# Kernel optimization log

Hardware: AMD Instinct MI355X
Metric: run time of the kernel (lower is better)

## Reference

```python
import jax, jax.numpy as jnp
import numpy as np

# dims: n_embd == dim_att == C, head_size N, heads H = C//N
B, T, C = 4, 2048, 2048
HS = 64
H = C // HS
D_MIX = 32
D_DECAY = 128
LAYER_ID, N_LAYER = 12, 24
LN_EPS = 1e-5


def setup_inputs() -> dict:
    key = jax.random.key(0)
    ks = jax.random.split(key, 12)
    r01 = LAYER_ID / (N_LAYER - 1)
    r1a0 = 1.0 - LAYER_ID / N_LAYER
    ddd = np.arange(C, dtype=np.float64) / C
    decay_speed = -6.0 + 5.0 * (np.arange(C, dtype=np.float64) / (C - 1)) ** (0.7 + 1.3 * r01)
    zig = ((np.arange(C) + 1) % 3 - 1) * 0.1
    faaaa = r01 * (1.0 - np.arange(C, dtype=np.float64) / (C - 1)) + zig
    uni = lambda k, sh, s: jax.random.uniform(k, sh, jnp.float32, -s, s)
    return dict(
        x_in=jax.random.normal(ks[0], (B, T, C), jnp.float32),
        shift_state=jax.random.normal(ks[1], (B, C), jnp.float32),
        wkv_state=jnp.zeros((B, H, HS, HS), jnp.float32),
        time_maa_r=jnp.asarray(1.0 - ddd ** (0.5 * r1a0), jnp.float32).reshape(1, 1, C),
        time_maa_k=jnp.asarray(1.0 - ddd ** r1a0, jnp.float32).reshape(1, 1, C),
        time_maa_v=jnp.asarray(1.0 - (ddd ** r1a0 + 0.3 * r01), jnp.float32).reshape(1, 1, C),
        time_maa_v2=jnp.asarray(1.0 - (ddd ** r1a0 + 0.3 * r01), jnp.float32).reshape(1, 1, C),
        time_maa_w1=uni(ks[2], (C, 4 * D_MIX), 0.01),  # zeros in true init; small values for nontrivial test
        time_maa_w2=uni(ks[3], (4, D_MIX, C), 0.01),
        time_maa_w=jnp.asarray(1.0 - ddd ** r1a0, jnp.float32).reshape(1, 1, C),
        time_maa_w_w1=uni(ks[4], (C, D_MIX), 0.01),
        time_maa_w_w2=uni(ks[5], (D_MIX, C), 0.01),
        time_decay=jnp.asarray(decay_speed, jnp.float32).reshape(1, 1, C),
        time_decay_w1=uni(ks[6], (C, D_DECAY), 0.01),
        time_decay_w2=uni(ks[7], (D_DECAY, C), 0.01),
        time_faaaa=jnp.asarray(faaaa, jnp.float32).reshape(H, HS),
        time_receptance=uni(ks[8], (C,), 1.0),
        time_key=uni(ks[9], (C,), 1.0),
        value_w=jax.random.normal(ks[10], (C, C), jnp.float32) / np.sqrt(C),
        output_w=jax.random.normal(ks[11], (C, C), jnp.float32) / np.sqrt(C),
        ln_gamma=jnp.ones((C,), jnp.float32),
        ln_beta=jnp.zeros((C,), jnp.float32),
    )


def _wkv6(r, k, v, decay, u, state):
    # r,k,v,decay: (B,T,H,N); u: (H,N); state: (B,H,N,N) [key i, value j]
    def step(S, inp):
        rt, kt, vt, dt = inp  # each (B,H,N)
        kv = kt[..., :, None] * vt[..., None, :]  # (B,H,N,N)
        y = jnp.einsum('bhi,bhij->bhj', rt, S + u[None, :, :, None] * kv)
        S = dt[..., None] * S + kv
        return S, y
    tb = lambda a: jnp.swapaxes(a, 0, 1)  # (B,T,...) -> (T,B,...)
    S_fin, ys = jax.lax.scan(step, state, (tb(r), tb(k), tb(v), tb(decay)))
    return tb(ys), S_fin  # (B,T,H,N), (B,H,N,N)


def reference(x_in, shift_state, wkv_state, time_maa_r, time_maa_k, time_maa_v,
              time_maa_v2, time_maa_w1, time_maa_w2, time_maa_w, time_maa_w_w1,
              time_maa_w_w2, time_decay, time_decay_w1, time_decay_w2, time_faaaa,
              time_receptance, time_key, value_w, output_w, ln_gamma, ln_beta):
    Bs, Ts, Cs = x_in.shape
    Hn, Nn = time_faaaa.shape
    # token-shift LoRA mixing coefficients (4, B, T, C)
    xxx = jnp.tanh(x_in @ time_maa_w1).reshape(Bs, Ts, 4, -1)
    mix = jnp.einsum('btfd,fdc->fbtc', xxx, time_maa_w2)
    x = x_in @ value_w.T  # value projection (B,T,C)
    shift_out = x[:, -1]
    dxprev = jnp.concatenate([shift_state[:, None, :], x[:, :-1]], axis=1) - x
    # data-dependent decay
    mw = jnp.tanh(x @ time_maa_w_w1) @ time_maa_w_w2
    xw = x + dxprev * (time_maa_w + mw)
    w = time_decay + jnp.tanh(xw @ time_decay_w1) @ time_decay_w2  # (B,T,C)
    mr, mk, mv, mv2 = mix[0], mix[1], mix[2], mix[3]
    xv = x + dxprev * (time_maa_v + mv)
    xr = x + dxprev * (time_maa_r + mr)
    xk = x + dxprev * (time_maa_k + mk)
    xv2 = x + dxprev * (time_maa_v2 + mv2)
    v = xv
    r = xr * time_receptance
    k = xk * time_key
    v2 = xv2
    decay = jnp.exp(-jnp.exp(w))  # per-channel decay in (0,1)
    k = k * (1.0 - decay)
    u = jnp.zeros_like(time_faaaa)
    hv = lambda a: a.reshape(Bs, Ts, Hn, Nn)
    y, S_fin = _wkv6(hv(r), hv(k), hv(v), hv(decay), u, wkv_state)
    y = y.reshape(Bs, Ts, Cs) + v2
    # LayerNorm over last dim
    mu = y.mean(-1, keepdims=True)
    var = ((y - mu) ** 2).mean(-1, keepdims=True)
    y = (y - mu) * jax.lax.rsqrt(var + LN_EPS) * ln_gamma + ln_beta
    out = y @ output_w.T
    return out
```

## Files before the change

kernel.cpp:

```cpp
#include <hip/hip_runtime.h>


#define Cdim 2048
#define Tdim 2048

using short8 = __attribute__((ext_vector_type(8))) short;
using f32x4  = __attribute__((ext_vector_type(4))) float;
using us4    = __attribute__((ext_vector_type(4))) unsigned short;
typedef unsigned short ushort_t;

__device__ __forceinline__ float b2f(unsigned short h) {
    union { unsigned int u; float f; } x; x.u = ((unsigned int)h) << 16; return x.f;
}
__device__ __forceinline__ unsigned short f2b(float f) {
    union { float f; unsigned int u; } x; x.f = f;
    unsigned int r = x.u + 0x7fffu + ((x.u >> 16) & 1u);
    return (unsigned short)(r >> 16);
}

__device__ __forceinline__ void gload16(const void* g, void* l) {
    __builtin_amdgcn_global_load_lds(
        (__attribute__((address_space(1))) void*)g,
        (__attribute__((address_space(3))) void*)l, 16, 0, 0);
}

__global__ __launch_bounds__(256) void prep_k(
    const float* __restrict__ x_in, const float* __restrict__ valw,
    const float* __restrict__ outw,
    ushort_t* __restrict__ xinB, ushort_t* __restrict__ valwB,
    ushort_t* __restrict__ outwB,
    const float* __restrict__ w1,  const float* __restrict__ ww1,
    const float* __restrict__ dw1, const float* __restrict__ dw2,
    const float* __restrict__ ww2, const float* __restrict__ w2,
    ushort_t* __restrict__ w1T,  ushort_t* __restrict__ ww1T,
    ushort_t* __restrict__ dw1T, ushort_t* __restrict__ dw2T,
    ushort_t* __restrict__ ww2T, ushort_t* __restrict__ w2T)
{
    size_t g = (size_t)blockIdx.x * 256 + threadIdx.x;
    if (g < 6291456) {
        const float* src; ushort_t* dst; size_t e;
        if (g < 4194304)      { src = x_in; dst = xinB;  e = g; }
        else if (g < 5242880) { src = valw; dst = valwB; e = g - 4194304; }
        else                  { src = outw; dst = outwB; e = g - 5242880; }
        const float4 v = ((const float4*)src)[e];
        us4 o; o.x = f2b(v.x); o.y = f2b(v.y); o.z = f2b(v.z); o.w = f2b(v.w);
        ((us4*)dst)[e] = o;
        return;
    }
    int idx = (int)(g - 6291456);
    if (idx < 262144) { int r = idx >> 7, c = idx & 127; w1T[c * 2048 + r] = f2b(w1[idx]); return; }
    idx -= 262144;
    if (idx < 65536)  { int r = idx >> 5, c = idx & 31;  ww1T[c * 2048 + r] = f2b(ww1[idx]); return; }
    idx -= 65536;
    if (idx < 262144) { int r = idx >> 7, c = idx & 127; dw1T[c * 2048 + r] = f2b(dw1[idx]); return; }
    idx -= 262144;
    if (idx < 262144) { int r = idx >> 11, c = idx & 2047; dw2T[c * 128 + r] = f2b(dw2[idx]); return; }
    idx -= 262144;
    if (idx < 65536)  { int r = idx >> 11, c = idx & 2047; ww2T[c * 32 + r] = f2b(ww2[idx]); return; }
    idx -= 65536;
    { int f = idx >> 16, rem = idx & 65535; int r = rem >> 11, c = rem & 2047;
      w2T[f * 65536 + c * 32 + r] = f2b(w2[idx]); }
}

template <int MODE>
__global__ __launch_bounds__(512, 2) void gemm256_k(
    const ushort_t* __restrict__ A,
    const ushort_t* __restrict__ Bw,
    ushort_t* __restrict__ outB,
    float* __restrict__ outF)
{
    __shared__ __align__(16) ushort_t lds[65536];

    const int tid  = threadIdx.x;
    const int wave = tid >> 6, lane = tid & 63;
    const int wm = wave >> 2, wn = wave & 3;
    const int fr = lane & 15, quad = lane >> 4;
    const int og8 = (((lane & 7) ^ ((lane >> 3) & 7)) * 8);

    const int id  = blockIdx.x;
    const int swz = (id & 7) * 32 + (id >> 3);
    const int mbase = (swz >> 3) * 256;
    const int nbase = (swz & 7) * 256;

    f32x4 acc[8][4];
#pragma unroll
    for (int i = 0; i < 8; ++i)
#pragma unroll
        for (int j = 0; j < 4; ++j)
#pragma unroll
            for (int r = 0; r < 4; ++r) acc[i][j][r] = 0.f;

    auto stage_half = [&](const ushort_t* __restrict__ G, int growb,
                          int dstb, int kt) {
#pragma unroll
        for (int i = 0; i < 2; ++i) {
            const int rh = i * 64 + wave * 8 + (lane >> 3);
            gload16(G + (size_t)(growb + rh) * Cdim + kt * 64 + og8,
                    &lds[dstb + (i * 512 + wave * 64) * 8]);
        }
    };

    short8 afr[4][2], bfr[2][2];

    auto LOADA = [&](int p, int mo) {
#pragma unroll
        for (int mi = 0; mi < 4; ++mi)
#pragma unroll
            for (int k = 0; k < 2; ++k) {
                const int row = wm * 128 + (mo + mi) * 16 + fr;
                afr[mi][k] = *(const short8*)
                    &lds[p + row * 64 + (((k * 4 + quad) ^ (fr & 7)) * 8)];
            }
    };
    auto LOADB = [&](int p, int no) {
#pragma unroll
        for (int ni = 0; ni < 2; ++ni)
#pragma unroll
            for (int k = 0; k < 2; ++k) {
                const int row = wn * 64 + (no + ni) * 16 + fr;
                bfr[ni][k] = *(const short8*)
                    &lds[32768 + p + row * 64 + (((k * 4 + quad) ^ (fr & 7)) * 8)];
            }
    };
    auto MFMA16 = [&](int mo, int no) {
        __builtin_amdgcn_s_setprio(1);
#pragma unroll
        for (int mi = 0; mi < 4; ++mi)
#pragma unroll
            for (int ni = 0; ni < 2; ++ni)
#pragma unroll
                for (int k = 0; k < 2; ++k)
                    acc[mo + mi][no + ni] = __builtin_amdgcn_mfma_f32_16x16x32_bf16(
                        afr[mi][k], bfr[ni][k], acc[mo + mi][no + ni], 0, 0, 0);
        __builtin_amdgcn_s_setprio(0);
    };

    stage_half(A,  mbase,       0,            0);
    stage_half(A,  mbase + 128, 8192,         0);
    stage_half(Bw, nbase,       32768,        0);
    stage_half(Bw, nbase + 128, 32768 + 8192, 0);

#pragma unroll 2
    for (int t = 0; t < 32; ++t) {
        const int p  = (t & 1) * 16384;
        const int q  = 16384 - p;
        const int kn = (t < 31) ? t + 1 : t;

        asm volatile("s_waitcnt vmcnt(0)\n\ts_barrier" ::: "memory");
        LOADA(p, 0); LOADB(p, 0);
        stage_half(A, mbase,       q,        kn);
        stage_half(A, mbase + 128, q + 8192, kn);
        asm volatile("s_barrier" ::: "memory");
        asm volatile("s_waitcnt lgkmcnt(0)" ::: "memory");
        MFMA16(0, 0);

        asm volatile("s_barrier" ::: "memory");
        LOADB(p, 2);
        stage_half(Bw, nbase,       32768 + q,        kn);
        stage_half(Bw, nbase + 128, 32768 + q + 8192, kn);
        asm volatile("s_barrier" ::: "memory");
        asm volatile("s_waitcnt lgkmcnt(0)" ::: "memory");
        MFMA16(0, 2);

        asm volatile("s_barrier" ::: "memory");
        LOADA(p, 4);
        asm volatile("s_barrier" ::: "memory");
        asm volatile("s_waitcnt lgkmcnt(0)" ::: "memory");
        MFMA16(4, 2);

        asm volatile("s_barrier" ::: "memory");
        LOADB(p, 0);
        asm volatile("s_barrier" ::: "memory");
        asm volatile("s_waitcnt lgkmcnt(0)" ::: "memory");
        MFMA16(4, 0);
    }

    const int row0 = mbase + wm * 128 + quad * 4;
    const int col0 = nbase + wn * 64 + fr;
#pragma unroll
    for (int mi = 0; mi < 8; ++mi)
#pragma unroll
        for (int ni = 0; ni < 4; ++ni)
#pragma unroll
            for (int r = 0; r < 4; ++r) {
                const int row = row0 + mi * 16 + r;
                const int col = col0 + ni * 16;
                const size_t idx = (size_t)row * Cdim + col;
                if constexpr (MODE == 2) outB[idx] = f2b(acc[mi][ni][r]);
                else                     outF[idx] = acc[mi][ni][r];
            }
}

__global__ __launch_bounds__(256) void mix5_k(
    const ushort_t* __restrict__ xxx,
    const ushort_t* __restrict__ mwpre,
    const ushort_t* __restrict__ w2T,
    const ushort_t* __restrict__ ww2T,
    const ushort_t* __restrict__ xB,
    const float*    __restrict__ shiftS,
    const float* __restrict__ maa_r, const float* __restrict__ maa_k,
    const float* __restrict__ maa_v, const float* __restrict__ maa_v2,
    const float* __restrict__ maa_w,
    const float* __restrict__ recep, const float* __restrict__ tkey,
    ushort_t* __restrict__ mR,  ushort_t* __restrict__ mK,
    ushort_t* __restrict__ mV,  ushort_t* __restrict__ mV2,
    ushort_t* __restrict__ xwB)
{
    __shared__ __align__(16) ushort_t xs[129 * 136];
    __shared__ __align__(16) ushort_t abuf[128 * 32];
    __shared__ __align__(16) ushort_t bbuf[128 * 32];

    const int tid  = threadIdx.x;
    const int wave = tid >> 6, lane = tid & 63;
    const int wm = wave >> 1, wn = wave & 1;
    const int fr = lane & 15, quad = lane >> 4;

    const int mbase = blockIdx.x * 128;
    const int nbase = blockIdx.y * 128;
    const int b  = mbase >> 11;
    const int t0 = mbase & 2047;

#pragma unroll
    for (int it = 0; it < 8; ++it) {
        const int idx = it * 256 + tid;
        const int r = idx >> 4, c8 = (idx & 15) * 8;
        *(short8*)&xs[(r + 1) * 136 + c8] =
            *(const short8*)&xB[(size_t)(mbase + r) * Cdim + nbase + c8];
    }
    if (tid < 128)
        xs[tid] = (t0 > 0) ? xB[(size_t)(mbase - 1) * Cdim + nbase + tid]
                           : f2b(shiftS[(size_t)b * Cdim + nbase + tid]);

    const ushort_t* asrc[5] = {xxx, xxx + 32, xxx + 64, xxx + 96, mwpre};
    const int       alda[5] = {128, 128, 128, 128, 32};
    const ushort_t* bsrc[5] = {w2T, w2T + 65536, w2T + 131072, w2T + 196608, ww2T};
    const float*    cvec[5] = {maa_r, maa_k, maa_v, maa_v2, maa_w};
    const float*    cmul[5] = {recep, tkey, nullptr, nullptr, nullptr};
    ushort_t*       outs[5] = {mR, mK, mV, mV2, xwB};

    auto stageAB = [&](int o) {
#pragma unroll
        for (int i = 0; i < 2; ++i) {
            const int slot = i * 256 + tid;
            const int r = slot >> 2, oct = slot & 3;
            const int sw = ((oct ^ (r & 3)) * 8);
            gload16(asrc[o] + (size_t)(mbase + r) * alda[o] + sw, &abuf[slot * 8]);
            gload16(bsrc[o] + (size_t)(nbase + r) * 32 + sw,      &bbuf[slot * 8]);
        }
    };

    stageAB(0);
    __syncthreads();

    const int row0l = wm * 64 + quad * 4;
    const int col0l = wn * 64 + fr;

#pragma unroll
    for (int o = 0; o < 5; ++o) {
        short8 af[4], bf[4];
#pragma unroll
        for (int mi = 0; mi < 4; ++mi) {
            const int r = wm * 64 + mi * 16 + fr;
            af[mi] = *(const short8*)&abuf[r * 32 + ((quad ^ (r & 3)) * 8)];
        }
#pragma unroll
        for (int ni = 0; ni < 4; ++ni) {
            const int r = wn * 64 + ni * 16 + fr;
            bf[ni] = *(const short8*)&bbuf[r * 32 + ((quad ^ (r & 3)) * 8)];
        }
        asm volatile("s_waitcnt lgkmcnt(0)" ::: "memory");
        __builtin_amdgcn_sched_barrier(0);
        asm volatile("s_barrier" ::: "memory");
        if (o < 4) stageAB(o + 1);

        f32x4 acc[4][4];
#pragma unroll
        for (int mi = 0; mi < 4; ++mi)
#pragma unroll
            for (int ni = 0; ni < 4; ++ni) {
#pragma unroll
                for (int r = 0; r < 4; ++r) acc[mi][ni][r] = 0.f;
                acc[mi][ni] = __builtin_amdgcn_mfma_f32_16x16x32_bf16(
                    af[mi], bf[ni], acc[mi][ni], 0, 0, 0);
            }

        const float* cv = cvec[o];
        const float* cm = cmul[o];
        ushort_t* op = outs[o];
#pragma unroll
        for (int mi = 0; mi < 4; ++mi)
#pragma unroll
            for (int ni = 0; ni < 4; ++ni)
#pragma unroll
                for (int r = 0; r < 4; ++r) {
                    const int lr = row0l + mi * 16 + r;
                    const int lc = col0l + ni * 16;
                    const int col = nbase + lc;
                    const float x  = b2f(xs[(lr + 1) * 136 + lc]);
                    const float xp = (lr == 0 && t0 == 0)
                                         ? shiftS[(size_t)b * Cdim + col]
                                         : b2f(xs[lr * 136 + lc]);
                    float val = x + (xp - x) * (cv[col] + acc[mi][ni][r]);
                    if (cm) val *= cm[col];
                    op[(size_t)(mbase + lr) * Cdim + col] = f2b(val);
                }
        if (o < 4)
            asm volatile("s_waitcnt vmcnt(0)\n\ts_barrier" ::: "memory");
    }
}

template <int MODE>
__global__ __launch_bounds__(256) void gemm_bt_k(
    const ushort_t* __restrict__ A, int lda,
    const ushort_t* __restrict__ Bw, int ldb,
    int N, int K,
    ushort_t* __restrict__ outB, int ldc,
    const float* __restrict__ cvec,
    ushort_t* __restrict__ inplace)
{
    __shared__ __align__(16) ushort_t At[128 * 32];
    __shared__ __align__(16) ushort_t Bt[128 * 32];

    const int tid  = threadIdx.x;
    const int wave = tid >> 6, lane = tid & 63;
    const int wm = wave >> 1, wn = wave & 1;
    const int fr = lane & 15, quad = lane >> 4;
    const int cr = lane >> 2;
    const int cc = (lane & 3) * 8;

    f32x4 acc[4][4];
#pragma unroll
    for (int i = 0; i < 4; ++i)
#pragma unroll
        for (int j = 0; j < 4; ++j)
#pragma unroll
            for (int r = 0; r < 4; ++r) acc[i][j][r] = 0.f;

    const int mbase = blockIdx.x * 128;
    const int nbase = blockIdx.y * 128;

    for (int k0 = 0; k0 < K; k0 += 32) {
        __syncthreads();
#pragma unroll
        for (int c2 = 0; c2 < 2; ++c2) {
            const int q  = wave * 2 + c2;
            const int ar = mbase + q * 16 + cr;
            gload16(A + (size_t)ar * lda + k0 + cc, &At[q * 512]);
            int br = nbase + q * 16 + cr;
            br = br < N ? br : N - 1;
            gload16(Bw + (size_t)br * ldb + k0 + cc, &Bt[q * 512]);
        }
        __syncthreads();

        short8 af[4], bfr[4];
#pragma unroll
        for (int mi = 0; mi < 4; ++mi)
            af[mi] = *(const short8*)&At[(wm * 64 + mi * 16 + fr) * 32 + quad * 8];
#pragma unroll
        for (int ni = 0; ni < 4; ++ni)
            bfr[ni] = *(const short8*)&Bt[(wn * 64 + ni * 16 + fr) * 32 + quad * 8];
#pragma unroll
        for (int mi = 0; mi < 4; ++mi)
#pragma unroll
            for (int ni = 0; ni < 4; ++ni)
                acc[mi][ni] = __builtin_amdgcn_mfma_f32_16x16x32_bf16(
                    af[mi], bfr[ni], acc[mi][ni], 0, 0, 0);
    }

    const int row0 = mbase + wm * 64 + quad * 4;
    const int col0 = nbase + wn * 64 + fr;
#pragma unroll
    for (int mi = 0; mi < 4; ++mi) {
#pragma unroll
        for (int ni = 0; ni < 4; ++ni) {
            const int col = col0 + ni * 16;
#pragma unroll
            for (int r = 0; r < 4; ++r) {
                const int row = row0 + mi * 16 + r;
                const float v = acc[mi][ni][r];
                const size_t idx = (size_t)row * ldc + col;
                if constexpr (MODE == 1) {
                    if (col < N) outB[idx] = f2b(tanhf(v));
                } else {
                    const float w  = cvec[col] + v;
                    const float ew = __expf(w);
                    outB[idx] = f2b(ew);
                    inplace[idx] = f2b(b2f(inplace[idx]) * (1.f - __expf(-ew)));
                }
            }
        }
    }
}

__global__ __launch_bounds__(64) void wkv_chunk_a(
    const ushort_t* __restrict__ ewB,
    ushort_t* rB, ushort_t* kB,
    const ushort_t* __restrict__ vB,
    ushort_t* __restrict__ uOut, float* __restrict__ dtot)
{
    const int c = blockIdx.x, h = blockIdx.y, b = blockIdx.z;
    const int lane = threadIdx.x;
    const int fr = lane & 15, quad = lane >> 4;
    __shared__ __align__(16) ushort_t kTT[64 * 40];
    __shared__ __align__(16) ushort_t vT [64 * 40];

    const size_t rowbase = ((size_t)b * Tdim + c * 32) * Cdim + h * 64;

    float Lrun = 0.f;
    for (int t = 0; t < 32; ++t) {
        const size_t off = rowbase + (size_t)t * Cdim + lane;
        const float e  = b2f(ewB[off]);
        const float rv = b2f(rB[off]);
        const float kv = b2f(kB[off]);
        const ushort_t rT = f2b(rv * __expf(Lrun));
        const ushort_t kT = f2b(kv * __expf(e - Lrun));
        rB[off] = rT;
        kB[off] = kT;
        kTT[lane * 40 + t] = kT;
        vT [lane * 40 + t] = vB[off];
        Lrun -= e;
    }
    const int slab = (b * 32 + h) * 64 + c;
    dtot[(size_t)slab * 64 + lane] = __expf(Lrun);
    __syncthreads();

    short8 af[4], bf[4];
#pragma unroll
    for (int mj = 0; mj < 4; ++mj)
        af[mj] = *(const short8*)&vT[(mj * 16 + fr) * 40 + quad * 8];
#pragma unroll
    for (int ni = 0; ni < 4; ++ni)
        bf[ni] = *(const short8*)&kTT[(ni * 16 + fr) * 40 + quad * 8];

    ushort_t* uo = uOut + (size_t)slab * 4096;
#pragma unroll
    for (int mj = 0; mj < 4; ++mj) {
#pragma unroll
        for (int ni = 0; ni < 4; ++ni) {
            f32x4 acc = {0.f, 0.f, 0.f, 0.f};
            acc = __builtin_amdgcn_mfma_f32_16x16x32_bf16(af[mj], bf[ni], acc, 0, 0, 0);
#pragma unroll
            for (int r = 0; r < 4; ++r) {
                const int j = mj * 16 + quad * 4 + r;
                const int i = ni * 16 + fr;
                uo[j * 64 + i] = f2b(acc[r]);
            }
        }
    }
}

__global__ __launch_bounds__(256) void wkv_scan_b(
    ushort_t* __restrict__ slabs, const float* __restrict__ dtot,
    const float* __restrict__ s0)
{
    const int jhi = blockIdx.x, h = blockIdx.y, b = blockIdx.z;
    const int tid = threadIdx.x;
    const int ip = tid & 31, jl = tid >> 5;
    const int i0 = ip * 2;
    const int j  = jhi * 8 + jl;
    const size_t bh = (size_t)(b * 32 + h);
    const size_t base = bh * 64;

    __shared__ float dsh[64 * 64];
    for (int e = tid; e < 4096; e += 256) dsh[e] = dtot[base * 64 + e];

    const float* sp = s0 + bh * 4096;
    float sa = sp[i0 * 64 + j];
    float sb = sp[(i0 + 1) * 64 + j];
    __syncthreads();

    unsigned int* up =
        (unsigned int*)(slabs + base * 4096 + (size_t)j * 64 + i0);
#pragma unroll 8
    for (int c = 0; c < 64; ++c) {
        const unsigned int u = up[(size_t)c * 2048];
        const float2 dt = *(const float2*)&dsh[c * 64 + i0];
        const unsigned int pre =
            (unsigned int)f2b(sa) | ((unsigned int)f2b(sb) << 16);
        sa = dt.x * (sa + b2f((ushort_t)(u & 0xffffu)));
        sb = dt.y * (sb + b2f((ushort_t)(u >> 16)));
        up[(size_t)c * 2048] = pre;
    }
}

__global__ __launch_bounds__(64) void wkv_chunk_c(
    const ushort_t* __restrict__ rB, const ushort_t* __restrict__ kB,
    ushort_t* vB, const ushort_t* __restrict__ slabs)
{
    const int c = blockIdx.x, h = blockIdx.y, b = blockIdx.z;
    const int lane = threadIdx.x;
    const int fr = lane & 15, quad = lane >> 4;
    __shared__ __align__(16) ushort_t rTs[32 * 64];
    __shared__ __align__(16) ushort_t kTs[32 * 64];
    __shared__ __align__(16) ushort_t vTs[64 * 40];
    __shared__ __align__(16) ushort_t Ams[32 * 32];

    const size_t rowbase = ((size_t)b * Tdim + c * 32) * Cdim + h * 64;

#pragma unroll
    for (int it = 0; it < 4; ++it) {
        const int idx = it * 64 + lane;
        const int t = idx >> 3, oct = idx & 7;
        const size_t g = rowbase + (size_t)t * Cdim + oct * 8;
        const int sw = ((oct ^ (t & 7)) * 8);
        *(short8*)&rTs[t * 64 + sw] = *(const short8*)&rB[g];
        *(short8*)&kTs[t * 64 + sw] = *(const short8*)&kB[g];
    }
    for (int t = 0; t < 32; ++t)
        vTs[lane * 40 + t] = vB[rowbase + (size_t)t * Cdim + lane];
    __syncthreads();

    f32x4 aacc[2][2];
#pragma unroll
    for (int mt = 0; mt < 2; ++mt)
#pragma unroll
        for (int st = 0; st < 2; ++st)
#pragma unroll
            for (int r = 0; r < 4; ++r) aacc[mt][st][r] = 0.f;

#pragma unroll
    for (int kk = 0; kk < 2; ++kk) {
        short8 ra[2], kb2[2];
#pragma unroll
        for (int mt = 0; mt < 2; ++mt) {
            const int t = mt * 16 + fr;
            ra[mt] = *(const short8*)&rTs[t * 64 + (((kk * 4 + quad) ^ (t & 7)) * 8)];
        }
#pragma unroll
        for (int st = 0; st < 2; ++st) {
            const int s = st * 16 + fr;
            kb2[st] = *(const short8*)&kTs[s * 64 + (((kk * 4 + quad) ^ (s & 7)) * 8)];
        }
#pragma unroll
        for (int mt = 0; mt < 2; ++mt)
#pragma unroll
            for (int st = 0; st < 2; ++st)
                aacc[mt][st] = __builtin_amdgcn_mfma_f32_16x16x32_bf16(
                    ra[mt], kb2[st], aacc[mt][st], 0, 0, 0);
    }

#pragma unroll
    for (int mt = 0; mt < 2; ++mt)
#pragma unroll
        for (int st = 0; st < 2; ++st)
#pragma unroll
            for (int r = 0; r < 4; ++r) {
                const int t = mt * 16 + quad * 4 + r;
                const int s = st * 16 + fr;
                Ams[t * 32 + s] = (t > s) ? f2b(aacc[mt][st][r]) : (ushort_t)0;
            }
    __syncthreads();

    f32x4 y[2][4];
#pragma unroll
    for (int mt = 0; mt < 2; ++mt)
#pragma unroll
        for (int nj = 0; nj < 4; ++nj)
#pragma unroll
            for (int r = 0; r < 4; ++r) y[mt][nj][r] = 0.f;

    {
        short8 aa[2], bb[4];
#pragma unroll
        for (int mt = 0; mt < 2; ++mt)
            aa[mt] = *(const short8*)&Ams[(mt * 16 + fr) * 32 + quad * 8];
#pragma unroll
        for (int nj = 0; nj < 4; ++nj)
            bb[nj] = *(const short8*)&vTs[(nj * 16 + fr) * 40 + quad * 8];
#pragma unroll
        for (int mt = 0; mt < 2; ++mt)
#pragma unroll
            for (int nj = 0; nj < 4; ++nj)
                y[mt][nj] = __builtin_amdgcn_mfma_f32_16x16x32_bf16(
                    aa[mt], bb[nj], y[mt][nj], 0, 0, 0);
    }
    const ushort_t* sl = slabs + (size_t)((b * 32 + h) * 64 + c) * 4096;
#pragma unroll
    for (int kk = 0; kk < 2; ++kk) {
        short8 aa[2], bb[4];
#pragma unroll
        for (int mt = 0; mt < 2; ++mt) {
            const int t = mt * 16 + fr;
            aa[mt] = *(const short8*)&rTs[t * 64 + (((kk * 4 + quad) ^ (t & 7)) * 8)];
        }
#pragma unroll
        for (int nj = 0; nj < 4; ++nj)
            bb[nj] = *(const short8*)&sl[(nj * 16 + fr) * 64 + kk * 32 + quad * 8];
#pragma unroll
        for (int mt = 0; mt < 2; ++mt)
#pragma unroll
            for (int nj = 0; nj < 4; ++nj)
                y[mt][nj] = __builtin_amdgcn_mfma_f32_16x16x32_bf16(
                    aa[mt], bb[nj], y[mt][nj], 0, 0, 0);
    }
#pragma unroll
    for (int mt = 0; mt < 2; ++mt)
#pragma unroll
        for (int nj = 0; nj < 4; ++nj)
#pragma unroll
            for (int r = 0; r < 4; ++r) {
                const int t = mt * 16 + quad * 4 + r;
                const int j = nj * 16 + fr;
                vB[rowbase + (size_t)t * Cdim + j] = f2b(y[mt][nj][r]);
            }
}

__global__ __launch_bounds__(256) void ln_k(
    const ushort_t* __restrict__ yB, const ushort_t* __restrict__ v2,
    const float* __restrict__ gamma, const float* __restrict__ beta,
    ushort_t* __restrict__ out)
{
    const size_t base = (size_t)blockIdx.x * Cdim;
    const int tid = threadIdx.x;
    const int wave = tid >> 6, lane = tid & 63;

    float sum = 0.f, sq = 0.f;
    for (int c = tid; c < Cdim; c += 256) {
        const float s = b2f(yB[base + c]) + b2f(v2[base + c]);
        sum += s; sq += s * s;
    }
#pragma unroll
    for (int o = 1; o < 64; o <<= 1) {
        sum += __shfl_xor(sum, o);
        sq  += __shfl_xor(sq, o);
    }
    __shared__ float red[8];
    if (lane == 0) { red[wave] = sum; red[4 + wave] = sq; }
    __syncthreads();
    sum = red[0] + red[1] + red[2] + red[3];
    sq  = red[4] + red[5] + red[6] + red[7];
    const float mu  = sum * (1.f / Cdim);
    const float var = sq * (1.f / Cdim) - mu * mu;
    const float rsd = rsqrtf(var + 1e-5f);
    for (int c = tid; c < Cdim; c += 256) {
        const float s = b2f(yB[base + c]) + b2f(v2[base + c]);
        out[base + c] = f2b((s - mu) * rsd * gamma[c] + beta[c]);
    }
}

extern "C" void kernel_launch(void* const* d_in, const int* in_sizes, int n_in,
                              void* d_out, int out_size, void* d_ws, size_t ws_size,
                              hipStream_t stream)
{
    (void)in_sizes; (void)n_in; (void)out_size; (void)ws_size;
    const float* x_in   = (const float*)d_in[0];
    const float* shiftS = (const float*)d_in[1];
    const float* wkvS   = (const float*)d_in[2];
    const float* maa_r  = (const float*)d_in[3];
    const float* maa_k  = (const float*)d_in[4];
    const float* maa_v  = (const float*)d_in[5];
    const float* maa_v2 = (const float*)d_in[6];
    const float* maa_w1 = (const float*)d_in[7];
    const float* maa_w2 = (const float*)d_in[8];
    const float* maa_w  = (const float*)d_in[9];
    const float* ww1    = (const float*)d_in[10];
    const float* ww2    = (const float*)d_in[11];
    const float* tdecay = (const float*)d_in[12];
    const float* dw1    = (const float*)d_in[13];
    const float* dw2    = (const float*)d_in[14];
    const float* recep  = (const float*)d_in[16];
    const float* tkey   = (const float*)d_in[17];
    const float* valw   = (const float*)d_in[18];
    const float* outw   = (const float*)d_in[19];
    const float* gamma  = (const float*)d_in[20];
    const float* beta   = (const float*)d_in[21];

    char* ws = (char*)d_ws;
    const size_t MB = 1ull << 20;
    ushort_t* xB    = (ushort_t*)(ws + 0 * MB);
    ushort_t* mR    = (ushort_t*)(ws + 32 * MB);
    ushort_t* mK    = (ushort_t*)(ws + 64 * MB);
    ushort_t* mV2   = (ushort_t*)(ws + 96 * MB);
    ushort_t* xinB  = (ushort_t*)(ws + 128 * MB);
    ushort_t* mV    = xinB;
    ushort_t* valwB = (ushort_t*)(ws + 160 * MB);
    ushort_t* outwB = (ushort_t*)(ws + 168 * MB);
    char* sm = ws + 176 * MB;
    ushort_t* xxx   = (ushort_t*)(sm + 0);
    ushort_t* mwpre = (ushort_t*)(sm + 2097152);
    ushort_t* gbuf  = (ushort_t*)(sm + 2621440);
    ushort_t* w1T   = (ushort_t*)(sm + 4718592);
    ushort_t* ww1T  = (ushort_t*)(sm + 5242880);
    ushort_t* dw1T  = (ushort_t*)(sm + 5373952);
    ushort_t* dw2T  = (ushort_t*)(sm + 5898240);
    ushort_t* ww2T  = (ushort_t*)(sm + 6422528);
    ushort_t* w2T   = (ushort_t*)(sm + 6553600);
    ushort_t* xwB   = (ushort_t*)d_out;
    ushort_t* ewB   = xB;
    ushort_t* slabs = (ushort_t*)d_out;
    float*    dtot  = (float*)xxx;

    const dim3 blk(256);
    const float* NF = nullptr;
    ushort_t* NUM = nullptr;
    float* NFM = nullptr;

    prep_k<<<dim3(29184), blk, 0, stream>>>(x_in, valw, outw, xinB, valwB, outwB,
                                            maa_w1, ww1, dw1, dw2, ww2, maa_w2,
                                            w1T, ww1T, dw1T, dw2T, ww2T, w2T);
    gemm256_k<2><<<dim3(256), dim3(512), 0, stream>>>(xinB, valwB, xB, NFM);
    gemm_bt_k<1><<<dim3(64, 1), blk, 0, stream>>>(xinB, 2048, w1T, 2048, 128, 2048,
                                                  xxx, 128, NF, NUM);
    gemm_bt_k<1><<<dim3(64, 1), blk, 0, stream>>>(xB, 2048, ww1T, 2048, 32, 2048,
                                                  mwpre, 32, NF, NUM);
    mix5_k<<<dim3(64, 16), blk, 0, stream>>>(xxx, mwpre, w2T, ww2T, xB, shiftS,
                                             maa_r, maa_k, maa_v, maa_v2, maa_w,
                                             recep, tkey, mR, mK, mV, mV2, xwB);
    gemm_bt_k<1><<<dim3(64, 1), blk, 0, stream>>>(xwB, 2048, dw1T, 2048, 128, 2048,
                                                  gbuf, 128, NF, NUM);
    gemm_bt_k<3><<<dim3(64, 16), blk, 0, stream>>>(gbuf, 128, dw2T, 128, 2048, 128,
                                                   ewB, 2048, tdecay, mK);
    wkv_chunk_a<<<dim3(64, 32, 4), dim3(64), 0, stream>>>(ewB, mR, mK, mV, slabs, dtot);
    wkv_scan_b<<<dim3(8, 32, 4),   blk,      0, stream>>>(slabs, dtot, wkvS);
    wkv_chunk_c<<<dim3(64, 32, 4), dim3(64), 0, stream>>>(mR, mK, mV, slabs);
    ln_k<<<dim3(8192), blk, 0, stream>>>(mV, mV2, gamma, beta, mR);
    gemm256_k<5><<<dim3(256), dim3(512), 0, stream>>>(mR, outwB, NUM, (float*)d_out);
}
```

Before: 699.1 us.

## Coalesce mix5 output stores via LDS staging and merge tanh projection GEMMs

The mix5 epilogue now writes each 64-row half of its output tile into an LDS staging buffer and then emits coalesced 16-byte row stores, replacing scattered 2-byte global stores. The wait before the next stage's barrier is relaxed from vmcnt(0) to vmcnt(8), so some outstanding loads can stay in flight. Two small tanh-projection GEMM launches are merged into one launch with a 2-wide y-grid, which halves the launch count and lets both run concurrently. The cost is extra LDS per block, which may lower occupancy, plus extra barriers in the epilogue.

```diff
diff --git a/kernel.cpp b/kernel.cpp
--- a/kernel.cpp
+++ b/kernel.cpp
@@ -209,6 +209,7 @@
     __shared__ __align__(16) ushort_t xs[129 * 136];
     __shared__ __align__(16) ushort_t abuf[128 * 32];
     __shared__ __align__(16) ushort_t bbuf[128 * 32];
+    __shared__ __align__(16) ushort_t outst[64 * 136];
 
     const int tid  = threadIdx.x;
     const int wave = tid >> 6, lane = tid & 63;
@@ -288,25 +289,118 @@
         const float* cm = cmul[o];
         ushort_t* op = outs[o];
 #pragma unroll
+        for (int h = 0; h < 2; ++h) {
+            if (wm == h) {
+#pragma unroll
+                for (int mi = 0; mi < 4; ++mi)
+#pragma unroll
+                    for (int ni = 0; ni < 4; ++ni) {
+                        const int lc = col0l + ni * 16;
+                        const int col = nbase + lc;
+#pragma unroll
+                        for (int r = 0; r < 4; ++r) {
+                            const int lr = row0l + mi * 16 + r;
+                            const float x  = b2f(xs[(lr + 1) * 136 + lc]);
+                            const float xp = (lr == 0 && t0 == 0)
+                                                 ? shiftS[(size_t)b * Cdim + col]
+                                                 : b2f(xs[lr * 136 + lc]);
+                            float val = x + (xp - x) * (cv[col] + acc[mi][ni][r]);
+                            if (cm) val *= cm[col];
+                            outst[(lr - h * 64) * 136 + lc] = f2b(val);
+                        }
+                    }
+            }
+            asm volatile("s_waitcnt lgkmcnt(0)" ::: "memory");
+            asm volatile("s_barrier" ::: "memory");
+#pragma unroll
+            for (int i = 0; i < 4; ++i) {
+                const int idx = i * 256 + tid;
+                const int row = idx >> 4, c8 = (idx & 15) * 8;
+                *(short8*)&op[(size_t)(mbase + h * 64 + row) * Cdim + nbase + c8] =
+                    *(const short8*)&outst[row * 136 + c8];
+            }
+            asm volatile("s_barrier" ::: "memory");
+        }
+        if (o < 4) {
+            asm volatile("s_waitcnt vmcnt(8)\n\ts_barrier" ::: "memory");
+        }
+    }
+}
+
+__global__ __launch_bounds__(256) void tanh2_k(
+    const ushort_t* __restrict__ xinB, const ushort_t* __restrict__ w1T,
+    const ushort_t* __restrict__ xB,   const ushort_t* __restrict__ ww1T,
+    ushort_t* __restrict__ xxx, ushort_t* __restrict__ mwpre)
+{
+    const int by = blockIdx.y;
+    const ushort_t* A  = by ? xB    : xinB;
+    const ushort_t* Bw = by ? ww1T  : w1T;
+    ushort_t* out      = by ? mwpre : xxx;
+    const int N        = by ? 32 : 128;
+    const int ldc      = N;
+
+    __shared__ __align__(16) ushort_t At[128 * 32];
+    __shared__ __align__(16) ushort_t Bt[128 * 32];
+
+    const int tid  = threadIdx.x;
+    const int wave = tid >> 6, lane = tid & 63;
+    const int wm = wave >> 1, wn = wave & 1;
+    const int fr = lane & 15, quad = lane >> 4;
+    const int cr = lane >> 2;
+    const int cc = (lane & 3) * 8;
+
+    f32x4 acc[4][4];
+#pragma unroll
+    for (int i = 0; i < 4; ++i)
+#pragma unroll
+        for (int j = 0; j < 4; ++j)
+#pragma unroll
+            for (int r = 0; r < 4; ++r) acc[i][j][r] = 0.f;
+
+    const int mbase = blockIdx.x * 128;
+
+    for (int k0 = 0; k0 < 2048; k0 += 32) {
+        __syncthreads();
+#pragma unroll
+        for (int c2 = 0; c2 < 2; ++c2) {
+            const int q  = wave * 2 + c2;
+            const int ar = mbase + q * 16 + cr;
+            gload16(A + (size_t)ar * 2048 + k0 + cc, &At[q * 512]);
+            int br = q * 16 + cr;
+            br = br < N ? br : N - 1;
+            gload16(Bw + (size_t)br * 2048 + k0 + cc, &Bt[q * 512]);
+        }
+        __syncthreads();
+
+        short8 af[4], bfr[4];
+#pragma unroll
         for (int mi = 0; mi < 4; ++mi)
+            af[mi] = *(const short8*)&At[(wm * 64 + mi * 16 + fr) * 32 + quad * 8];
+#pragma unroll
+        for (int ni = 0; ni < 4; ++ni)
+            bfr[ni] = *(const short8*)&Bt[(wn * 64 + ni * 16 + fr) * 32 + quad * 8];
+#pragma unroll
+        for (int mi = 0; mi < 4; ++mi)
 #pragma unroll
             for (int ni = 0; ni < 4; ++ni)
-#pragma unroll
-                for (int r = 0; r < 4; ++r) {
-                    const int lr = row0l + mi * 16 + r;
-                    const int lc = col0l + ni * 16;
-                    const int col = nbase + lc;
-                    const float x  = b2f(xs[(lr + 1) * 136 + lc]);
-                    const float xp = (lr == 0 && t0 == 0)
-                                         ? shiftS[(size_t)b * Cdim + col]
-                                         : b2f(xs[lr * 136 + lc]);
-                    float val = x + (xp - x) * (cv[col] + acc[mi][ni][r]);
-                    if (cm) val *= cm[col];
-                    op[(size_t)(mbase + lr) * Cdim + col] = f2b(val);
-                }
-        if (o < 4)
-            asm volatile("s_waitcnt vmcnt(0)\n\ts_barrier" ::: "memory");
-    }
+                acc[mi][ni] = __builtin_amdgcn_mfma_f32_16x16x32_bf16(
+                    af[mi], bfr[ni], acc[mi][ni], 0, 0, 0);
+    }
+
+    const int row0 = mbase + wm * 64 + quad * 4;
+    const int col0 = wn * 64 + fr;
+#pragma unroll
+    for (int mi = 0; mi < 4; ++mi)
+#pragma unroll
+        for (int ni = 0; ni < 4; ++ni) {
+            const int col = col0 + ni * 16;
+#pragma unroll
+            for (int r = 0; r < 4; ++r) {
+                const int row = row0 + mi * 16 + r;
+                if (col < N)
+                    out[(size_t)row * ldc + col] = f2b(tanhf(acc[mi][ni][r]));
+            }
+        }
 }
 
 template <int MODE>
@@ -699,10 +793,7 @@
                                             maa_w1, ww1, dw1, dw2, ww2, maa_w2,
                                             w1T, ww1T, dw1T, dw2T, ww2T, w2T);
     gemm256_k<2><<<dim3(256), dim3(512), 0, stream>>>(xinB, valwB, xB, NFM);
-    gemm_bt_k<1><<<dim3(64, 1), blk, 0, stream>>>(xinB, 2048, w1T, 2048, 128, 2048,
-                                                  xxx, 128, NF, NUM);
-    gemm_bt_k<1><<<dim3(64, 1), blk, 0, stream>>>(xB, 2048, ww1T, 2048, 32, 2048,
-                                                  mwpre, 32, NF, NUM);
+    tanh2_k<<<dim3(64, 2), blk, 0, stream>>>(xinB, w1T, xB, ww1T, xxx, mwpre);
     mix5_k<<<dim3(64, 16), blk, 0, stream>>>(xxx, mwpre, w2T, ww2T, xB, shiftS,
                                              maa_r, maa_k, maa_v, maa_v2, maa_w,
                                              recep, tkey, mR, mK, mV, mV2, xwB);
```

Measured after the change: 748.9 us. 7.1% more time.
